# Kernel optimization log

Hardware: AMD Instinct MI355X
Metric: run time of the kernel (lower is better)

## Reference

```python
import jax, jax.numpy as jnp
import numpy as np

# Static config matching init_kwargs
K0, K1 = 3, 3          # kernel_size
S0, S1 = 1, 1          # stride
P0, P1 = 1, 1          # padding
L_IN, L_OUT = 4, 8     # capsule lengths
ITERS = 3              # routing iterations


def setup_inputs() -> dict:
    key = jax.random.key(0)
    kx, kw = jax.random.split(key)
    x = jax.random.normal(kx, (4, 32, 56, 56), dtype=jnp.float32)
    # weight: (out_channels//out_length, in_channels//in_length * kH*kW, in_length, out_length)
    weight = jax.random.normal(kw, (8, 8 * K0 * K1, L_IN, L_OUT), dtype=jnp.float32)
    return {"x": x, "weight": weight}


def squash(t, axis=-1):
    norm = jnp.linalg.norm(t, axis=axis, keepdims=True)
    return (norm / (1.0 + norm ** 2)) * t


def reference(x, weight):
    N, C, H, W = x.shape
    H_out = 1 + (H + 2 * P0 - K0) // S0
    W_out = 1 + (W + 2 * P1 - K1) // S1
    G_in = C // L_IN
    G_out = weight.shape[0]
    kk = K0 * K1

    xp = jnp.pad(x, ((0, 0), (0, 0), (P0, P0), (P1, P1)))
    # im2col: stack kernel offsets (k0-major, k1-minor, matching torch unfold order)
    patches = jnp.stack(
        [xp[:, :, i:i + S0 * H_out:S0, j:j + S1 * W_out:S1]
         for i in range(K0) for j in range(K1)], axis=0)          # (kk, N, C, Ho, Wo)
    patches = patches.reshape(kk, N, G_in, L_IN, H_out, W_out)
    # -> (N, P, G_in, kk, L_in) with P = Ho*Wo
    xwin = jnp.transpose(patches, (1, 4, 5, 2, 0, 3)).reshape(
        N, H_out * W_out, G_in, kk, L_IN)

    w = weight.reshape(G_out, G_in, kk, L_IN, L_OUT)
    # priors: (G_out, N, P, G_in, kk, L_out)
    priors = jnp.einsum('npgkl,cgklm->cnpgkm', xwin, w)

    # dynamic routing
    logits = jnp.zeros_like(priors)
    v = None
    for r in range(ITERS):
        probs = jax.nn.softmax(logits, axis=-2)                    # over kk dim
        s = jnp.sum(probs * priors, axis=(-3, -2), keepdims=True)  # sum over G_in, kk
        v = squash(s, axis=-1)                                     # (G_out,N,P,1,1,L_out)
        if r != ITERS - 1:
            logits = logits + jnp.sum(priors * v, axis=-1, keepdims=True)

    out = v[:, :, :, 0, 0, :]                  # (G_out, N, P, L_out)
    out = jnp.transpose(out, (1, 0, 3, 2))     # (N, G_out, L_out, P)
    return out.reshape(N, G_out * L_OUT, H_out, W_out)
```

## Files before the change

kernel.cpp:

```cpp
#include <hip/hip_runtime.h>

#define NB   4
#define CIN  32
#define HH   56
#define WW   56
#define GOUT 8
#define LIN  4
#define LOUT 8
#define KK   9
#define HW   (HH * WW)
#define PIXTOT (NB * HW)
#define PPB  32
#define WSLICE 2304
#define WS_G 292
#define HP   58
#define WP   58

typedef float v2f __attribute__((ext_vector_type(2)));
typedef float v4f __attribute__((ext_vector_type(4)));

static __device__ __forceinline__ v2f fma2(v2f a, v2f b, v2f c) {
    return __builtin_elementwise_fma(a, b, c);
}

#define DPP_XADD(x, CTRL) \
    (x) += __int_as_float(__builtin_amdgcn_update_dpp( \
        0, __float_as_int(x), (CTRL), 0xF, 0xF, true))

__global__ __launch_bounds__(256) void transpose_x_kernel(
    const float* __restrict__ x, float* __restrict__ xt)
{
    __shared__ float tile[CIN * 57];
    const int b = blockIdx.x;
    const int n = b / HP;
    const int hp = b - n * HP;
    const int h = hp - 1;
    const int tid = threadIdx.x;
    const bool rowok = (unsigned)h < (unsigned)HH;

    if (rowok) {
        for (int i = tid; i < CIN * WW; i += 256) {
            const int ch = i / WW;
            const int w  = i - ch * WW;
            tile[ch * 57 + w] = x[((n * CIN + ch) * HH + h) * WW + w];
        }
    }
    __syncthreads();
    float* dst = xt + ((size_t)(n * HP + hp) * WP) * CIN;
    for (int i = tid; i < WP * CIN; i += 256) {
        const int wp = i >> 5;
        const int ch = i & 31;
        const bool ok = rowok && (wp >= 1) && (wp <= WW);
        dst[i] = ok ? tile[ch * 57 + (wp - 1)] : 0.0f;
    }
}

__global__ __launch_bounds__(256, 4) void caps_routing_kernel(
    const float* __restrict__ xt, const float* __restrict__ wt,
    float* __restrict__ out)
{
    __shared__ __align__(16) float ws[8 * WS_G];

    const int tid = threadIdx.x;
    const int c = blockIdx.y;

    const int g    = tid & 7;
    const int slot = tid >> 3;
    const int pix = blockIdx.x * PPB + slot;
    const int n = pix / HW;
    const int p = pix - n * HW;
    const int h = p / WW;
    const int w = p - h * WW;

    v4f xv4[KK];
    const float* base = xt + ((size_t)((n * HP + h) * WP + w)) * CIN + g * 4;
    #pragma unroll
    for (int ki = 0; ki < 3; ++ki)
        #pragma unroll
        for (int kj = 0; kj < 3; ++kj)
            xv4[ki * 3 + kj] =
                *reinterpret_cast<const v4f*>(base + (ki * WP + kj) * CIN);

    {
        const int gg = tid >> 5;
        const int r0 = tid & 31;
        const float* src = wt + c * WSLICE + gg * 288;
        float* dst = ws + gg * WS_G;
        #pragma unroll
        for (int j = 0; j < 9; ++j)
            dst[r0 + j * 32] = src[r0 + j * 32];
    }
    __syncthreads();

    v2f pr2[KK][4];
    v2f ks2[4] = {v2f{0.f,0.f}, v2f{0.f,0.f}, v2f{0.f,0.f}, v2f{0.f,0.f}};

    const float* wg = &ws[g * WS_G];
    #pragma unroll
    for (int k = 0; k < KK; ++k) {
        v2f a0 = {0.f,0.f}, a1 = {0.f,0.f}, a2 = {0.f,0.f}, a3 = {0.f,0.f};
        #pragma unroll
        for (int l = 0; l < LIN; ++l) {
            const float xs = xv4[k][l];
            const v2f xs2 = {xs, xs};
            const v4f w01 = *reinterpret_cast<const v4f*>(wg + k * 32 + l * 8);
            const v4f w23 = *reinterpret_cast<const v4f*>(wg + k * 32 + l * 8 + 4);
            a0 = fma2(xs2, __builtin_shufflevector(w01, w01, 0, 1), a0);
            a1 = fma2(xs2, __builtin_shufflevector(w01, w01, 2, 3), a1);
            a2 = fma2(xs2, __builtin_shufflevector(w23, w23, 0, 1), a2);
            a3 = fma2(xs2, __builtin_shufflevector(w23, w23, 2, 3), a3);
        }
        pr2[k][0] = a0; pr2[k][1] = a1; pr2[k][2] = a2; pr2[k][3] = a3;
        ks2[0] += a0; ks2[1] += a1; ks2[2] += a2; ks2[3] += a3;
    }

    float logits[KK];
    #pragma unroll
    for (int k = 0; k < KK; ++k) logits[k] = 0.0f;

    v2f vv[4];
    #pragma unroll
    for (int it = 0; it < 3; ++it) {
        v2f s2[4];
        if (it == 0) {
            #pragma unroll
            for (int j = 0; j < 4; ++j) s2[j] = ks2[j] * (1.0f / 9.0f);
        } else {
            float e[KK];
            float sum = 0.0f;
            #pragma unroll
            for (int k = 0; k < KK; ++k) { e[k] = __expf(logits[k]); sum += e[k]; }
            const float inv = 1.0f / sum;
            #pragma unroll
            for (int j = 0; j < 4; ++j) s2[j] = v2f{0.f, 0.f};
            #pragma unroll
            for (int k = 0; k < KK; ++k) {
                const v2f ek = {e[k], e[k]};
                #pragma unroll
                for (int j = 0; j < 4; ++j) s2[j] = fma2(ek, pr2[k][j], s2[j]);
            }
            const v2f inv2 = {inv, inv};
            #pragma unroll
            for (int j = 0; j < 4; ++j) s2[j] *= inv2;
        }

        #pragma unroll
        for (int j = 0; j < 4; ++j) { DPP_XADD(s2[j].x, 0xB1); DPP_XADD(s2[j].y, 0xB1); }
        #pragma unroll
        for (int j = 0; j < 4; ++j) { DPP_XADD(s2[j].x, 0x4E); DPP_XADD(s2[j].y, 0x4E); }
        #pragma unroll
        for (int j = 0; j < 4; ++j) { DPP_XADD(s2[j].x, 0x141); DPP_XADD(s2[j].y, 0x141); }

        v2f tq = s2[0] * s2[0];
        tq = fma2(s2[1], s2[1], tq);
        tq = fma2(s2[2], s2[2], tq);
        tq = fma2(s2[3], s2[3], tq);
        const float n2 = tq.x + tq.y;
        const float f = n2 * __builtin_amdgcn_rsqf(fmaxf(n2, 1e-30f))
                           * __builtin_amdgcn_rcpf(1.0f + n2);
        const v2f f2 = {f, f};
        #pragma unroll
        for (int j = 0; j < 4; ++j) vv[j] = f2 * s2[j];

        if (it != 2) {
            #pragma unroll
            for (int k = 0; k < KK; ++k) {
                v2f d2 = pr2[k][0] * vv[0];
                d2 = fma2(pr2[k][1], vv[1], d2);
                d2 = fma2(pr2[k][2], vv[2], d2);
                d2 = fma2(pr2[k][3], vv[3], d2);
                logits[k] += d2.x + d2.y;
            }
        }
    }

    const float vs[8] = { vv[0].x, vv[0].y, vv[1].x, vv[1].y,
                          vv[2].x, vv[2].y, vv[3].x, vv[3].y };
    float outv = vs[0];
    #pragma unroll
    for (int m = 1; m < LOUT; ++m) if (g == m) outv = vs[m];
    out[(n * GOUT * LOUT + c * LOUT + g) * HW + p] = outv;
}

extern "C" void kernel_launch(void* const* d_in, const int* in_sizes, int n_in,
                              void* d_out, int out_size, void* d_ws, size_t ws_size,
                              hipStream_t stream) {
    const float* x  = (const float*)d_in[0];
    const float* wt = (const float*)d_in[1];
    float* out = (float*)d_out;
    float* xt = (float*)d_ws;

    transpose_x_kernel<<<dim3(NB * HP), dim3(256), 0, stream>>>(x, xt);
    dim3 grid(PIXTOT / PPB, GOUT);
    caps_routing_kernel<<<grid, dim3(256), 0, stream>>>(xt, wt, out);
}
```

Measured before the change: 30.92 us.

## Fuse input transpose into routing kernel via per-row LDS halo tile

Removes the separate transpose/pad kernel and instead has each block (one output row, one output capsule group) load a 3-row halo of NCHW input directly into LDS in channel-last padded layout. Block size changes to 448 threads covering a full 56-pixel row. This removes one launch and the global round trip through the workspace. In exchange, every output-group block (8 per row) reloads the same input rows with strided, poorly coalesced reads. The larger block and LDS footprint may also reduce occupancy.

```diff
diff --git a/kernel.cpp b/kernel.cpp
--- a/kernel.cpp
+++ b/kernel.cpp
@@ -5,16 +5,15 @@
 #define HH   56
 #define WW   56
 #define GOUT 8
-#define LIN  4
 #define LOUT 8
 #define KK   9
 #define HW   (HH * WW)
-#define PIXTOT (NB * HW)
-#define PPB  32
 #define WSLICE 2304
 #define WS_G 292
-#define HP   58
-#define WP   58
+#define XCOLS 58
+#define XCH  36
+#define XTOT (3 * XCOLS * CIN)
+#define THREADS 448
 
 typedef float v2f __attribute__((ext_vector_type(2)));
 typedef float v4f __attribute__((ext_vector_type(4)));
@@ -27,61 +26,35 @@
     (x) += __int_as_float(__builtin_amdgcn_update_dpp( \
         0, __float_as_int(x), (CTRL), 0xF, 0xF, true))
 
-__global__ __launch_bounds__(256) void transpose_x_kernel(
-    const float* __restrict__ x, float* __restrict__ xt)
-{
-    __shared__ float tile[CIN * 57];
-    const int b = blockIdx.x;
-    const int n = b / HP;
-    const int hp = b - n * HP;
-    const int h = hp - 1;
-    const int tid = threadIdx.x;
-    const bool rowok = (unsigned)h < (unsigned)HH;
-
-    if (rowok) {
-        for (int i = tid; i < CIN * WW; i += 256) {
-            const int ch = i / WW;
-            const int w  = i - ch * WW;
-            tile[ch * 57 + w] = x[((n * CIN + ch) * HH + h) * WW + w];
-        }
-    }
-    __syncthreads();
-    float* dst = xt + ((size_t)(n * HP + hp) * WP) * CIN;
-    for (int i = tid; i < WP * CIN; i += 256) {
-        const int wp = i >> 5;
-        const int ch = i & 31;
-        const bool ok = rowok && (wp >= 1) && (wp <= WW);
-        dst[i] = ok ? tile[ch * 57 + (wp - 1)] : 0.0f;
-    }
-}
-
-__global__ __launch_bounds__(256, 4) void caps_routing_kernel(
-    const float* __restrict__ xt, const float* __restrict__ wt,
+__global__ __launch_bounds__(THREADS, 7) void caps_fused_kernel(
+    const float* __restrict__ x, const float* __restrict__ wt,
     float* __restrict__ out)
 {
-    __shared__ __align__(16) float ws[8 * WS_G];
+    __shared__ float ws[8 * WS_G];
+    __shared__ __align__(16) float xs[3 * XCOLS * XCH];
 
     const int tid = threadIdx.x;
     const int c = blockIdx.y;
+    const int rr = blockIdx.x;
+    const int n = rr / HH;
+    const int h = rr - n * HH;
 
-    const int g    = tid & 7;
-    const int slot = tid >> 3;
-    const int pix = blockIdx.x * PPB + slot;
-    const int n = pix / HW;
-    const int p = pix - n * HW;
-    const int h = p / WW;
-    const int w = p - h * WW;
+    const int g = tid & 7;
+    const int w = tid >> 3;
 
-    v4f xv4[KK];
-    const float* base = xt + ((size_t)((n * HP + h) * WP + w)) * CIN + g * 4;
-    #pragma unroll
-    for (int ki = 0; ki < 3; ++ki)
-        #pragma unroll
-        for (int kj = 0; kj < 3; ++kj)
-            xv4[ki * 3 + kj] =
-                *reinterpret_cast<const v4f*>(base + (ki * WP + kj) * CIN);
+    const float* xn = x + (size_t)n * CIN * HW;
+    for (int i = tid; i < XTOT; i += THREADS) {
+        const int seg = i / XCOLS;
+        const int col = i - seg * XCOLS;
+        const int ch  = seg & 31;
+        const int row = seg >> 5;
+        const int hh  = h - 1 + row;
+        const int wc  = col - 1;
+        const bool ok = ((unsigned)hh < (unsigned)HH) && ((unsigned)wc < (unsigned)WW);
+        xs[(row * XCOLS + col) * XCH + ch] = ok ? xn[ch * HW + hh * WW + wc] : 0.0f;
+    }
 
-    {
+    if (tid < 256) {
         const int gg = tid >> 5;
         const int r0 = tid & 31;
         const float* src = wt + c * WSLICE + gg * 288;
@@ -92,6 +65,14 @@
     }
     __syncthreads();
 
+    v4f xv4[KK];
+    #pragma unroll
+    for (int ki = 0; ki < 3; ++ki)
+        #pragma unroll
+        for (int kj = 0; kj < 3; ++kj)
+            xv4[ki * 3 + kj] = *reinterpret_cast<const v4f*>(
+                &xs[((ki * XCOLS) + (w + kj)) * XCH + g * 4]);
+
     v2f pr2[KK][4];
     v2f ks2[4] = {v2f{0.f,0.f}, v2f{0.f,0.f}, v2f{0.f,0.f}, v2f{0.f,0.f}};
 
@@ -100,9 +81,9 @@
     for (int k = 0; k < KK; ++k) {
         v2f a0 = {0.f,0.f}, a1 = {0.f,0.f}, a2 = {0.f,0.f}, a3 = {0.f,0.f};
         #pragma unroll
-        for (int l = 0; l < LIN; ++l) {
-            const float xs = xv4[k][l];
-            const v2f xs2 = {xs, xs};
+        for (int l = 0; l < 4; ++l) {
+            const float xsv = xv4[k][l];
+            const v2f xs2 = {xsv, xsv};
             const v4f w01 = *reinterpret_cast<const v4f*>(wg + k * 32 + l * 8);
             const v4f w23 = *reinterpret_cast<const v4f*>(wg + k * 32 + l * 8 + 4);
             a0 = fma2(xs2, __builtin_shufflevector(w01, w01, 0, 1), a0);
@@ -179,7 +160,7 @@
     float outv = vs[0];
     #pragma unroll
     for (int m = 1; m < LOUT; ++m) if (g == m) outv = vs[m];
-    out[(n * GOUT * LOUT + c * LOUT + g) * HW + p] = outv;
+    out[(n * GOUT * LOUT + c * LOUT + g) * HW + h * WW + w] = outv;
 }
 
 extern "C" void kernel_launch(void* const* d_in, const int* in_sizes, int n_in,
@@ -188,9 +169,7 @@
     const float* x  = (const float*)d_in[0];
     const float* wt = (const float*)d_in[1];
     float* out = (float*)d_out;
-    float* xt = (float*)d_ws;
 
-    transpose_x_kernel<<<dim3(NB * HP), dim3(256), 0, stream>>>(x, xt);
-    dim3 grid(PIXTOT / PPB, GOUT);
-    caps_routing_kernel<<<grid, dim3(256), 0, stream>>>(xt, wt, out);
+    dim3 grid(NB * HH, GOUT);
+    caps_fused_kernel<<<grid, dim3(THREADS), 0, stream>>>(x, wt, out);
 }
```

After: 105.0 us. 240% more time.

## Map one routing block per output row with 448 threads

Applied to the files above, without the earlier changes.

Each routing block now covers one full output row (56 pixels × 8 lanes = 448 threads) instead of 32 pixels, which cuts the block count and the number of redundant weight-slice loads into shared memory. The first iteration's 1/9 scale is folded into the squash factor, and the softmax reciprocal now uses the hardware rcp. Occupancy hints change from 4 to 2 blocks per CU, and the larger blocks add some register and occupancy risk.

```diff
diff --git a/kernel.cpp b/kernel.cpp
--- a/kernel.cpp
+++ b/kernel.cpp
@@ -5,16 +5,14 @@
 #define HH   56
 #define WW   56
 #define GOUT 8
-#define LIN  4
 #define LOUT 8
 #define KK   9
 #define HW   (HH * WW)
-#define PIXTOT (NB * HW)
-#define PPB  32
 #define WSLICE 2304
 #define WS_G 292
 #define HP   58
 #define WP   58
+#define THREADS 448
 
 typedef float v2f __attribute__((ext_vector_type(2)));
 typedef float v4f __attribute__((ext_vector_type(4)));
@@ -55,7 +53,7 @@
     }
 }
 
-__global__ __launch_bounds__(256, 4) void caps_routing_kernel(
+__global__ __launch_bounds__(THREADS, 2) void caps_routing_kernel(
     const float* __restrict__ xt, const float* __restrict__ wt,
     float* __restrict__ out)
 {
@@ -63,14 +61,12 @@
 
     const int tid = threadIdx.x;
     const int c = blockIdx.y;
+    const int rr = blockIdx.x;
+    const int n = rr / HH;
+    const int h = rr - n * HH;
 
-    const int g    = tid & 7;
-    const int slot = tid >> 3;
-    const int pix = blockIdx.x * PPB + slot;
-    const int n = pix / HW;
-    const int p = pix - n * HW;
-    const int h = p / WW;
-    const int w = p - h * WW;
+    const int g = tid & 7;
+    const int w = tid >> 3;
 
     v4f xv4[KK];
     const float* base = xt + ((size_t)((n * HP + h) * WP + w)) * CIN + g * 4;
@@ -81,7 +77,7 @@
             xv4[ki * 3 + kj] =
                 *reinterpret_cast<const v4f*>(base + (ki * WP + kj) * CIN);
 
-    {
+    if (tid < 256) {
         const int gg = tid >> 5;
         const int r0 = tid & 31;
         const float* src = wt + c * WSLICE + gg * 288;
@@ -100,9 +96,9 @@
     for (int k = 0; k < KK; ++k) {
         v2f a0 = {0.f,0.f}, a1 = {0.f,0.f}, a2 = {0.f,0.f}, a3 = {0.f,0.f};
         #pragma unroll
-        for (int l = 0; l < LIN; ++l) {
-            const float xs = xv4[k][l];
-            const v2f xs2 = {xs, xs};
+        for (int l = 0; l < 4; ++l) {
+            const float xsv = xv4[k][l];
+            const v2f xs2 = {xsv, xsv};
             const v4f w01 = *reinterpret_cast<const v4f*>(wg + k * 32 + l * 8);
             const v4f w23 = *reinterpret_cast<const v4f*>(wg + k * 32 + l * 8 + 4);
             a0 = fma2(xs2, __builtin_shufflevector(w01, w01, 0, 1), a0);
@@ -122,15 +118,17 @@
     #pragma unroll
     for (int it = 0; it < 3; ++it) {
         v2f s2[4];
+        float pre;
         if (it == 0) {
             #pragma unroll
-            for (int j = 0; j < 4; ++j) s2[j] = ks2[j] * (1.0f / 9.0f);
+            for (int j = 0; j < 4; ++j) s2[j] = ks2[j];
+            pre = 1.0f / 9.0f;
         } else {
             float e[KK];
             float sum = 0.0f;
             #pragma unroll
             for (int k = 0; k < KK; ++k) { e[k] = __expf(logits[k]); sum += e[k]; }
-            const float inv = 1.0f / sum;
+            const float inv = __builtin_amdgcn_rcpf(sum);
             #pragma unroll
             for (int j = 0; j < 4; ++j) s2[j] = v2f{0.f, 0.f};
             #pragma unroll
@@ -142,6 +140,7 @@
             const v2f inv2 = {inv, inv};
             #pragma unroll
             for (int j = 0; j < 4; ++j) s2[j] *= inv2;
+            pre = 1.0f;
         }
 
         #pragma unroll
@@ -155,12 +154,13 @@
         tq = fma2(s2[1], s2[1], tq);
         tq = fma2(s2[2], s2[2], tq);
         tq = fma2(s2[3], s2[3], tq);
-        const float n2 = tq.x + tq.y;
+        const float n2 = (tq.x + tq.y) * (pre * pre);
         const float f = n2 * __builtin_amdgcn_rsqf(fmaxf(n2, 1e-30f))
                            * __builtin_amdgcn_rcpf(1.0f + n2);
-        const v2f f2 = {f, f};
+        const float q = f * pre;
+        const v2f q2 = {q, q};
         #pragma unroll
-        for (int j = 0; j < 4; ++j) vv[j] = f2 * s2[j];
+        for (int j = 0; j < 4; ++j) vv[j] = q2 * s2[j];
 
         if (it != 2) {
             #pragma unroll
@@ -179,7 +179,7 @@
     float outv = vs[0];
     #pragma unroll
     for (int m = 1; m < LOUT; ++m) if (g == m) outv = vs[m];
-    out[(n * GOUT * LOUT + c * LOUT + g) * HW + p] = outv;
+    out[(n * GOUT * LOUT + c * LOUT + g) * HW + h * WW + w] = outv;
 }
 
 extern "C" void kernel_launch(void* const* d_in, const int* in_sizes, int n_in,
@@ -191,6 +191,6 @@
     float* xt = (float*)d_ws;
 
     transpose_x_kernel<<<dim3(NB * HP), dim3(256), 0, stream>>>(x, xt);
-    dim3 grid(PIXTOT / PPB, GOUT);
-    caps_routing_kernel<<<grid, dim3(256), 0, stream>>>(xt, wt, out);
+    dim3 grid(NB * HH, GOUT);
+    caps_routing_kernel<<<grid, dim3(THREADS), 0, stream>>>(xt, wt, out);
 }
```

After: 30.75 us, median of 3. Within noise of the previous version (-0.6%).

## Split each capsule's output vector across two lanes with 512-thread blocks

Applied to the files above, without the earlier changes.

Each (pixel, input group) is now handled by two lanes, each computing four of the eight output components, and blocks grow to 512 threads. The weight slice is re-laid out in shared memory per half. Cross-group reductions use shuffle-xor instead of DPP, and each lane pair combines partial norms and dot products with one extra shuffle. The aim is fewer registers per thread and more parallelism to hide latency. The cost is that every x load is duplicated across the lane pair, more shuffle traffic, and half the lanes stay idle during the store.

```diff
diff --git a/kernel.cpp b/kernel.cpp
--- a/kernel.cpp
+++ b/kernel.cpp
@@ -5,27 +5,22 @@
 #define HH   56
 #define WW   56
 #define GOUT 8
-#define LIN  4
 #define LOUT 8
 #define KK   9
 #define HW   (HH * WW)
 #define PIXTOT (NB * HW)
 #define PPB  32
 #define WSLICE 2304
-#define WS_G 292
+#define WS_S 148
 #define HP   58
 #define WP   58
+#define THREADS 512
 
-typedef float v2f __attribute__((ext_vector_type(2)));
 typedef float v4f __attribute__((ext_vector_type(4)));
 
-static __device__ __forceinline__ v2f fma2(v2f a, v2f b, v2f c) {
+static __device__ __forceinline__ v4f fma4(v4f a, v4f b, v4f c) {
     return __builtin_elementwise_fma(a, b, c);
 }
-
-#define DPP_XADD(x, CTRL) \
-    (x) += __int_as_float(__builtin_amdgcn_update_dpp( \
-        0, __float_as_int(x), (CTRL), 0xF, 0xF, true))
 
 __global__ __launch_bounds__(256) void transpose_x_kernel(
     const float* __restrict__ x, float* __restrict__ xt)
@@ -55,18 +50,20 @@
     }
 }
 
-__global__ __launch_bounds__(256, 4) void caps_routing_kernel(
+__global__ __launch_bounds__(THREADS, 2) void caps_routing_kernel(
     const float* __restrict__ xt, const float* __restrict__ wt,
     float* __restrict__ out)
 {
-    __shared__ __align__(16) float ws[8 * WS_G];
+    __shared__ __align__(16) float ws[16 * WS_S];
 
     const int tid = threadIdx.x;
     const int c = blockIdx.y;
 
-    const int g    = tid & 7;
-    const int slot = tid >> 3;
-    const int pix = blockIdx.x * PPB + slot;
+    const int q   = tid & 15;
+    const int g   = q >> 1;
+    const int mh  = q & 1;
+    const int pl  = tid >> 4;
+    const int pix = blockIdx.x * PPB + pl;
     const int n = pix / HW;
     const int p = pix - n * HW;
     const int h = p / WW;
@@ -82,104 +79,97 @@
                 *reinterpret_cast<const v4f*>(base + (ki * WP + kj) * CIN);
 
     {
-        const int gg = tid >> 5;
-        const int r0 = tid & 31;
-        const float* src = wt + c * WSLICE + gg * 288;
-        float* dst = ws + gg * WS_G;
-        #pragma unroll
-        for (int j = 0; j < 9; ++j)
-            dst[r0 + j * 32] = src[r0 + j * 32];
+        const float* wc = wt + c * WSLICE;
+        for (int i = tid; i < 2304; i += THREADS) {
+            const int g2 = i / 144;
+            const int r  = i - g2 * 144;
+            const int k  = r >> 4;
+            const int l  = (r >> 2) & 3;
+            const int mi = r & 3;
+            ws[g2 * WS_S + r] =
+                wc[(g2 >> 1) * 288 + k * 32 + l * 8 + (g2 & 1) * 4 + mi];
+        }
     }
     __syncthreads();
 
-    v2f pr2[KK][4];
-    v2f ks2[4] = {v2f{0.f,0.f}, v2f{0.f,0.f}, v2f{0.f,0.f}, v2f{0.f,0.f}};
-
-    const float* wg = &ws[g * WS_G];
+    v4f pr4[KK];
+    v4f ks4 = {0.f, 0.f, 0.f, 0.f};
+    const float* wg = &ws[q * WS_S];
     #pragma unroll
     for (int k = 0; k < KK; ++k) {
-        v2f a0 = {0.f,0.f}, a1 = {0.f,0.f}, a2 = {0.f,0.f}, a3 = {0.f,0.f};
-        #pragma unroll
-        for (int l = 0; l < LIN; ++l) {
-            const float xs = xv4[k][l];
-            const v2f xs2 = {xs, xs};
-            const v4f w01 = *reinterpret_cast<const v4f*>(wg + k * 32 + l * 8);
-            const v4f w23 = *reinterpret_cast<const v4f*>(wg + k * 32 + l * 8 + 4);
-            a0 = fma2(xs2, __builtin_shufflevector(w01, w01, 0, 1), a0);
-            a1 = fma2(xs2, __builtin_shufflevector(w01, w01, 2, 3), a1);
-            a2 = fma2(xs2, __builtin_shufflevector(w23, w23, 0, 1), a2);
-            a3 = fma2(xs2, __builtin_shufflevector(w23, w23, 2, 3), a3);
-        }
-        pr2[k][0] = a0; pr2[k][1] = a1; pr2[k][2] = a2; pr2[k][3] = a3;
-        ks2[0] += a0; ks2[1] += a1; ks2[2] += a2; ks2[3] += a3;
+        const v4f* w4 = reinterpret_cast<const v4f*>(wg + k * 16);
+        const v4f wl0 = w4[0], wl1 = w4[1], wl2 = w4[2], wl3 = w4[3];
+        v4f a = v4f{xv4[k][0], xv4[k][0], xv4[k][0], xv4[k][0]} * wl0;
+        a = fma4(v4f{xv4[k][1], xv4[k][1], xv4[k][1], xv4[k][1]}, wl1, a);
+        a = fma4(v4f{xv4[k][2], xv4[k][2], xv4[k][2], xv4[k][2]}, wl2, a);
+        a = fma4(v4f{xv4[k][3], xv4[k][3], xv4[k][3], xv4[k][3]}, wl3, a);
+        pr4[k] = a;
+        ks4 += a;
     }
 
     float logits[KK];
     #pragma unroll
     for (int k = 0; k < KK; ++k) logits[k] = 0.0f;
 
-    v2f vv[4];
+    v4f vv4;
     #pragma unroll
     for (int it = 0; it < 3; ++it) {
-        v2f s2[4];
+        v4f s4;
+        float pre;
         if (it == 0) {
-            #pragma unroll
-            for (int j = 0; j < 4; ++j) s2[j] = ks2[j] * (1.0f / 9.0f);
+            s4 = ks4;
+            pre = 1.0f / 9.0f;
         } else {
             float e[KK];
             float sum = 0.0f;
             #pragma unroll
             for (int k = 0; k < KK; ++k) { e[k] = __expf(logits[k]); sum += e[k]; }
-            const float inv = 1.0f / sum;
+            const float inv = __builtin_amdgcn_rcpf(sum);
+            s4 = v4f{0.f, 0.f, 0.f, 0.f};
             #pragma unroll
-            for (int j = 0; j < 4; ++j) s2[j] = v2f{0.f, 0.f};
-            #pragma unroll
-            for (int k = 0; k < KK; ++k) {
-                const v2f ek = {e[k], e[k]};
-                #pragma unroll
-                for (int j = 0; j < 4; ++j) s2[j] = fma2(ek, pr2[k][j], s2[j]);
-            }
-            const v2f inv2 = {inv, inv};
-            #pragma unroll
-            for (int j = 0; j < 4; ++j) s2[j] *= inv2;
+            for (int k = 0; k < KK; ++k)
+                s4 = fma4(v4f{e[k], e[k], e[k], e[k]}, pr4[k], s4);
+            const v4f inv4 = {inv, inv, inv, inv};
+            s4 *= inv4;
+            pre = 1.0f;
         }
 
         #pragma unroll
-        for (int j = 0; j < 4; ++j) { DPP_XADD(s2[j].x, 0xB1); DPP_XADD(s2[j].y, 0xB1); }
-        #pragma unroll
-        for (int j = 0; j < 4; ++j) { DPP_XADD(s2[j].x, 0x4E); DPP_XADD(s2[j].y, 0x4E); }
-        #pragma unroll
-        for (int j = 0; j < 4; ++j) { DPP_XADD(s2[j].x, 0x141); DPP_XADD(s2[j].y, 0x141); }
+        for (int off = 2; off <= 8; off <<= 1) {
+            #pragma unroll
+            for (int j = 0; j < 4; ++j)
+                s4[j] += __shfl_xor(s4[j], off, 64);
+        }
 
-        v2f tq = s2[0] * s2[0];
-        tq = fma2(s2[1], s2[1], tq);
-        tq = fma2(s2[2], s2[2], tq);
-        tq = fma2(s2[3], s2[3], tq);
-        const float n2 = tq.x + tq.y;
+        float n2p = s4[0] * s4[0];
+        n2p = fmaf(s4[1], s4[1], n2p);
+        n2p = fmaf(s4[2], s4[2], n2p);
+        n2p = fmaf(s4[3], s4[3], n2p);
+        const float n2full = n2p + __shfl_xor(n2p, 1, 64);
+        const float n2 = n2full * (pre * pre);
         const float f = n2 * __builtin_amdgcn_rsqf(fmaxf(n2, 1e-30f))
                            * __builtin_amdgcn_rcpf(1.0f + n2);
-        const v2f f2 = {f, f};
-        #pragma unroll
-        for (int j = 0; j < 4; ++j) vv[j] = f2 * s2[j];
+        const float qsc = f * pre;
+        vv4 = v4f{qsc, qsc, qsc, qsc} * s4;
 
         if (it != 2) {
             #pragma unroll
             for (int k = 0; k < KK; ++k) {
-                v2f d2 = pr2[k][0] * vv[0];
-                d2 = fma2(pr2[k][1], vv[1], d2);
-                d2 = fma2(pr2[k][2], vv[2], d2);
-                d2 = fma2(pr2[k][3], vv[3], d2);
-                logits[k] += d2.x + d2.y;
+                float d = pr4[k][0] * vv4[0];
+                d = fmaf(pr4[k][1], vv4[1], d);
+                d = fmaf(pr4[k][2], vv4[2], d);
+                d = fmaf(pr4[k][3], vv4[3], d);
+                logits[k] += d + __shfl_xor(d, 1, 64);
             }
         }
     }
 
-    const float vs[8] = { vv[0].x, vv[0].y, vv[1].x, vv[1].y,
-                          vv[2].x, vv[2].y, vv[3].x, vv[3].y };
-    float outv = vs[0];
-    #pragma unroll
-    for (int m = 1; m < LOUT; ++m) if (g == m) outv = vs[m];
-    out[(n * GOUT * LOUT + c * LOUT + g) * HW + p] = outv;
+    if (mh == (g >> 2)) {
+        float outv = vv4[0];
+        #pragma unroll
+        for (int mi = 1; mi < 4; ++mi) if ((g & 3) == mi) outv = vv4[mi];
+        out[(n * GOUT * LOUT + c * LOUT + g) * HW + p] = outv;
+    }
 }
 
 extern "C" void kernel_launch(void* const* d_in, const int* in_sizes, int n_in,
@@ -192,5 +182,5 @@
 
     transpose_x_kernel<<<dim3(NB * HP), dim3(256), 0, stream>>>(x, xt);
     dim3 grid(PIXTOT / PPB, GOUT);
-    caps_routing_kernel<<<grid, dim3(256), 0, stream>>>(xt, wt, out);
+    caps_routing_kernel<<<grid, dim3(THREADS), 0, stream>>>(xt, wt, out);
 }
```

Result: slower. 40.01 us (+29.4%).
